# Kernel tuning notes

Measured on AMD Instinct MI355X. Metric: run time of the kernel, lower is better.

## Reference

```python
import jax, jax.numpy as jnp
import numpy as np

B, N, D, H, DEG = 2, 20000, 256, 8, 8
E = N * DEG
EPS = 1e-3  # keras LayerNormalization default epsilon


def layer_norm(x, gamma, beta):
    mu = jnp.mean(x, axis=-1, keepdims=True)
    var = jnp.mean(jnp.square(x - mu), axis=-1, keepdims=True)
    return (x - mu) * jax.lax.rsqrt(var + EPS) * gamma + beta


def setup_inputs() -> dict:
    key = jax.random.key(0)
    ks = jax.random.split(key, 8)
    x = jax.random.normal(ks[0], (B, N, D), dtype=jnp.float32)
    # edge list sorted by source node; every node has DEG out-edges so
    # segment_sum covers all N segments (matches tf.math.segment_sum semantics)
    src = jnp.repeat(jnp.arange(N, dtype=jnp.int64), DEG)
    dst = jax.random.randint(ks[1], (E,), 0, N, dtype=jnp.int64)
    edges = jnp.stack([src, dst], axis=1)  # [E, 2]
    scale = 0.05
    wq = jax.random.normal(ks[2], (D, D), dtype=jnp.float32) * scale
    wk = jax.random.normal(ks[3], (D, D), dtype=jnp.float32) * scale
    wv = jax.random.normal(ks[4], (D, D), dtype=jnp.float32) * scale
    wo = jax.random.normal(ks[5], (D, D), dtype=jnp.float32) * scale
    zeros = jnp.zeros((D,), dtype=jnp.float32)
    ones = jnp.ones((D,), dtype=jnp.float32)
    return {
        "x": x, "edges": edges,
        "wq": wq, "bq": zeros, "wk": wk, "bk": zeros,
        "wv": wv, "bv": zeros, "wo": wo, "bo": zeros,
        "gamma1": ones, "beta1": zeros, "gamma2": ones, "beta2": zeros,
    }


def reference(x, edges, wq, bq, wk, bk, wv, bv, wo, bo, gamma1, beta1, gamma2, beta2):
    b, n, d = x.shape
    h, dh = H, D // H
    xn = layer_norm(x, gamma1, beta1)                      # [B,N,D]
    # QKV projections, split heads, move node axis to front: [N,B,H,dh]
    def proj(w, bias):
        y = (xn @ w + bias).reshape(b, n, h, dh)
        return jnp.transpose(y, (1, 0, 2, 3))
    q, k, v = proj(wq, bq), proj(wk, bk), proj(wv, bv)
    src, dst = edges[:, 0], edges[:, 1]
    q_part = q[src]                                         # [E,B,H,dh]
    k_part = k[dst]
    v_part = v[dst]
    logits = jnp.sum(q_part * k_part, axis=-1, keepdims=True) / jnp.sqrt(
        jnp.asarray(dh, dtype=x.dtype))                     # [E,B,H,1]
    w = jnp.exp(logits)                                     # unnormalized softmax (as in source)
    num = jax.ops.segment_sum(v_part * w, src, num_segments=n)  # [N,B,H,dh]
    den = jax.ops.segment_sum(w, src, num_segments=n)           # [N,B,H,1]
    attn = num / den
    attn = jnp.transpose(attn, (1, 0, 2, 3)).reshape(b, n, d)   # [B,N,D]
    concat = xn + attn                                      # residual uses normed input (source reassigns `inputs`)
    out = layer_norm(concat, gamma2, beta2)
    out = jax.nn.relu(out @ wo + bo)
    return out + concat
```

## Files before the change

kernel.cpp:

```cpp
#include <hip/hip_runtime.h>


typedef __bf16 bf16x8 __attribute__((ext_vector_type(8)));
typedef float  f32x4  __attribute__((ext_vector_type(4)));

__device__ __forceinline__ float bf2f(unsigned short u) {
    union { unsigned int i; float f; } v; v.i = ((unsigned int)u) << 16; return v.f;
}
__device__ __forceinline__ unsigned short f2bf(float f) {
    union { float f; unsigned int i; } v; v.f = f;
    unsigned int x = v.i;
    unsigned int r = (x + 0x7FFFu + ((x >> 16) & 1u)) >> 16;
    return (unsigned short)r;
}

#define NNODE 20000
#define ROWS  40000
#define DMODEL 256

__global__ __launch_bounds__(256) void prep_kernel(
    const float* __restrict__ wq, const float* __restrict__ wk,
    const float* __restrict__ wv, const float* __restrict__ wo,
    const float* __restrict__ bq, const float* __restrict__ bk,
    const float* __restrict__ bv, const float* __restrict__ bo,
    unsigned short* __restrict__ Wqkvt,
    unsigned short* __restrict__ Wot,
    float* __restrict__ biasq,
    float* __restrict__ biaso)
{
    int idx = blockIdx.x * 256 + threadIdx.x;
    if (idx < 768 * 256) {
        int n = idx >> 8, k = idx & 255;
        int sel = n >> 8, nl = n & 255;
        const float* w = (sel == 0) ? wq : (sel == 1) ? wk : wv;
        Wqkvt[idx] = f2bf(w[k * 256 + nl]);
    } else {
        int idx2 = idx - 768 * 256;
        int n = idx2 >> 8, k = idx2 & 255;
        Wot[idx2] = f2bf(wo[k * 256 + n]);
    }
    if (idx < 768) {
        const float* bb = (idx < 256) ? bq : (idx < 512) ? bk : bv;
        biasq[idx] = bb[idx & 255];
    }
    if (idx >= 768 && idx < 1024) biaso[idx - 768] = bo[idx - 768];
}

__global__ __launch_bounds__(256) void ln1_kernel(
    const float* __restrict__ x,
    const float* __restrict__ g1, const float* __restrict__ b1,
    unsigned short* __restrict__ xn)
{
    int wave = threadIdx.x >> 6, lane = threadIdx.x & 63;
    int sub = lane >> 5, hl = lane & 31;
    int m = blockIdx.x * 8 + wave * 2 + sub;
    const float* xp = x + (size_t)m * DMODEL + hl * 8;
    float4 x0 = *(const float4*)xp;
    float4 x1 = *(const float4*)(xp + 4);
    float f[8] = {x0.x, x0.y, x0.z, x0.w, x1.x, x1.y, x1.z, x1.w};
    float s = 0.f, ss = 0.f;
    #pragma unroll
    for (int t = 0; t < 8; ++t) { s += f[t]; ss += f[t]*f[t]; }
    #pragma unroll
    for (int mk = 1; mk < 32; mk <<= 1) { s += __shfl_xor(s, mk); ss += __shfl_xor(ss, mk); }
    float mu  = s * (1.f/256.f);
    float var = ss * (1.f/256.f) - mu*mu;
    float rs  = rsqrtf(var + 1e-3f);
    float4 g0 = *(const float4*)(g1 + hl * 8);
    float4 g1v = *(const float4*)(g1 + hl * 8 + 4);
    float4 b0 = *(const float4*)(b1 + hl * 8);
    float4 b1v = *(const float4*)(b1 + hl * 8 + 4);
    float gg[8] = {g0.x, g0.y, g0.z, g0.w, g1v.x, g1v.y, g1v.z, g1v.w};
    float bb[8] = {b0.x, b0.y, b0.z, b0.w, b1v.x, b1v.y, b1v.z, b1v.w};
    unsigned short o[8];
    #pragma unroll
    for (int t = 0; t < 8; ++t) o[t] = f2bf((f[t] - mu) * rs * gg[t] + bb[t]);
    *(int4*)(xn + (size_t)m * DMODEL + hl * 8) = *(const int4*)o;
}

#define LDS_W 72
#define MFMA_BF16(d, a, b) d = __builtin_amdgcn_mfma_f32_16x16x32_bf16(a, b, d, 0, 0, 0)

template<bool EPI>
__global__ __launch_bounds__(256, 2) void gemm_kernel(
    const unsigned short* __restrict__ A,
    const unsigned short* __restrict__ Bt,
    const float* __restrict__ bias,
    void* __restrict__ C,
    const unsigned short* __restrict__ resid,
    int M, int Ncols)
{
    __shared__ unsigned short As[128 * LDS_W];
    __shared__ unsigned short Bs[128 * LDS_W];
    int tid  = threadIdx.x;
    int wave = tid >> 6, lane = tid & 63;
    int quad = lane >> 4, l16 = lane & 15;
    int m0 = blockIdx.x * 128, n0 = blockIdx.y * 128;
    int wm = (wave >> 1) * 64, wn = (wave & 1) * 64;

    int srow = tid >> 1;
    int sseg = (tid & 1) * 32;
    int arow = m0 + srow; if (arow >= M) arow = M - 1;
    const unsigned short* ArowP = A  + (size_t)arow * 256 + sseg;
    const unsigned short* BrowP = Bt + (size_t)(n0 + srow) * 256 + sseg;
    unsigned short* AsP = &As[srow * LDS_W + sseg];
    unsigned short* BsP = &Bs[srow * LDS_W + sseg];

    f32x4 acc00 = {}, acc01 = {}, acc02 = {}, acc03 = {};
    f32x4 acc10 = {}, acc11 = {}, acc12 = {}, acc13 = {};
    f32x4 acc20 = {}, acc21 = {}, acc22 = {}, acc23 = {};
    f32x4 acc30 = {}, acc31 = {}, acc32 = {}, acc33 = {};

    for (int kt = 0; kt < 4; ++kt) {
        const unsigned short* ap = ArowP + kt * 64;
        const unsigned short* bp = BrowP + kt * 64;
        int4 va0 = *(const int4*)(ap);
        int4 va1 = *(const int4*)(ap + 8);
        int4 va2 = *(const int4*)(ap + 16);
        int4 va3 = *(const int4*)(ap + 24);
        int4 vb0 = *(const int4*)(bp);
        int4 vb1 = *(const int4*)(bp + 8);
        int4 vb2 = *(const int4*)(bp + 16);
        int4 vb3 = *(const int4*)(bp + 24);
        __syncthreads();
        *(int4*)(AsP)      = va0;
        *(int4*)(AsP + 8)  = va1;
        *(int4*)(AsP + 16) = va2;
        *(int4*)(AsP + 24) = va3;
        *(int4*)(BsP)      = vb0;
        *(int4*)(BsP + 8)  = vb1;
        *(int4*)(BsP + 16) = vb2;
        *(int4*)(BsP + 24) = vb3;
        __syncthreads();
        #pragma unroll
        for (int ks = 0; ks < 64; ks += 32) {
            bf16x8 a0 = *(const bf16x8*)&As[(wm +  0 + l16) * LDS_W + ks + quad * 8];
            bf16x8 a1 = *(const bf16x8*)&As[(wm + 16 + l16) * LDS_W + ks + quad * 8];
            bf16x8 a2 = *(const bf16x8*)&As[(wm + 32 + l16) * LDS_W + ks + quad * 8];
            bf16x8 a3 = *(const bf16x8*)&As[(wm + 48 + l16) * LDS_W + ks + quad * 8];
            bf16x8 b0 = *(const bf16x8*)&Bs[(wn +  0 + l16) * LDS_W + ks + quad * 8];
            bf16x8 b1 = *(const bf16x8*)&Bs[(wn + 16 + l16) * LDS_W + ks + quad * 8];
            bf16x8 b2 = *(const bf16x8*)&Bs[(wn + 32 + l16) * LDS_W + ks + quad * 8];
            bf16x8 b3 = *(const bf16x8*)&Bs[(wn + 48 + l16) * LDS_W + ks + quad * 8];
            MFMA_BF16(acc00, a0, b0); MFMA_BF16(acc01, a0, b1);
            MFMA_BF16(acc02, a0, b2); MFMA_BF16(acc03, a0, b3);
            MFMA_BF16(acc10, a1, b0); MFMA_BF16(acc11, a1, b1);
            MFMA_BF16(acc12, a1, b2); MFMA_BF16(acc13, a1, b3);
            MFMA_BF16(acc20, a2, b0); MFMA_BF16(acc21, a2, b1);
            MFMA_BF16(acc22, a2, b2); MFMA_BF16(acc23, a2, b3);
            MFMA_BF16(acc30, a3, b0); MFMA_BF16(acc31, a3, b1);
            MFMA_BF16(acc32, a3, b2); MFMA_BF16(acc33, a3, b3);
        }
    }

#define EPI_STORE(accv, R, CC) do {                                          \
        int col = n0 + wn + (CC) * 16 + l16;                                 \
        float bb = bias[col];                                                \
        int rowb = m0 + wm + (R) * 16 + quad * 4;                            \
        _Pragma("unroll")                                                    \
        for (int rr = 0; rr < 4; ++rr) {                                     \
            int row = rowb + rr;                                             \
            if (row < M) {                                                   \
                float v = (accv)[rr] + bb;                                   \
                if (EPI) {                                                   \
                    v = fmaxf(v, 0.f);                                       \
                    v += bf2f(resid[(size_t)row * 256 + col]);               \
                    ((float*)C)[(size_t)row * Ncols + col] = v;              \
                } else {                                                     \
                    ((unsigned short*)C)[(size_t)row * Ncols + col] = f2bf(v);\
                }                                                            \
            }                                                                \
        }                                                                    \
    } while (0)

    EPI_STORE(acc00, 0, 0); EPI_STORE(acc01, 0, 1); EPI_STORE(acc02, 0, 2); EPI_STORE(acc03, 0, 3);
    EPI_STORE(acc10, 1, 0); EPI_STORE(acc11, 1, 1); EPI_STORE(acc12, 1, 2); EPI_STORE(acc13, 1, 3);
    EPI_STORE(acc20, 2, 0); EPI_STORE(acc21, 2, 1); EPI_STORE(acc22, 2, 2); EPI_STORE(acc23, 2, 3);
    EPI_STORE(acc30, 3, 0); EPI_STORE(acc31, 3, 1); EPI_STORE(acc32, 3, 2); EPI_STORE(acc33, 3, 3);
#undef EPI_STORE
}

__global__ __launch_bounds__(256) void attn_kernel(
    const unsigned short* __restrict__ qkv,
    const int* __restrict__ edges,
    const unsigned short* __restrict__ xn,
    const float* __restrict__ g2, const float* __restrict__ b2,
    unsigned short* __restrict__ concat,
    unsigned short* __restrict__ h2)
{
    int wave = threadIdx.x >> 6, lane = threadIdx.x & 63;
    int i = blockIdx.x * 4 + wave;
    int b = lane >> 5, hl = lane & 31;
    size_t m = (size_t)b * NNODE + i;

    int4 qi = *(const int4*)(qkv + m * 768 + hl * 8);
    const unsigned short* qs = (const unsigned short*)&qi;
    float qf[8];
    #pragma unroll
    for (int t = 0; t < 8; ++t) qf[t] = bf2f(qs[t]);

    int jv = 0;
    if (lane < 8) jv = edges[2 * (i * 8 + lane) + 1];

    float acc[8] = {};
    float den = 0.f;
    const float scale = 0.17677669529663687f;
    #pragma unroll
    for (int e = 0; e < 8; ++e) {
        int j = __shfl(jv, e);
        const unsigned short* kp = qkv + ((size_t)b * NNODE + j) * 768 + 256 + hl * 8;
        int4 ki = *(const int4*)kp;
        int4 vi = *(const int4*)(kp + 256);
        const unsigned short* ks = (const unsigned short*)&ki;
        const unsigned short* vs = (const unsigned short*)&vi;
        float dot = 0.f;
        #pragma unroll
        for (int t = 0; t < 8; ++t) dot += qf[t] * bf2f(ks[t]);
        dot += __shfl_xor(dot, 1);
        dot += __shfl_xor(dot, 2);
        float w = __expf(dot * scale);
        #pragma unroll
        for (int t = 0; t < 8; ++t) acc[t] += w * bf2f(vs[t]);
        den += w;
    }
    float inv = 1.f / den;

    int4 xi = *(const int4*)(xn + m * DMODEL + hl * 8);
    const unsigned short* xs = (const unsigned short*)&xi;
    float c[8], s = 0.f, ss = 0.f;
    #pragma unroll
    for (int t = 0; t < 8; ++t) { c[t] = bf2f(xs[t]) + acc[t] * inv; s += c[t]; ss += c[t]*c[t]; }
    #pragma unroll
    for (int mk = 1; mk < 32; mk <<= 1) { s += __shfl_xor(s, mk); ss += __shfl_xor(ss, mk); }
    float mu  = s * (1.f/256.f);
    float var = ss * (1.f/256.f) - mu*mu;
    float rs  = rsqrtf(var + 1e-3f);

    float4 ga = *(const float4*)(g2 + hl * 8);
    float4 gb = *(const float4*)(g2 + hl * 8 + 4);
    float4 ba = *(const float4*)(b2 + hl * 8);
    float4 bb = *(const float4*)(b2 + hl * 8 + 4);
    float gg[8] = {ga.x, ga.y, ga.z, ga.w, gb.x, gb.y, gb.z, gb.w};
    float bv[8] = {ba.x, ba.y, ba.z, ba.w, bb.x, bb.y, bb.z, bb.w};
    unsigned short oc[8], oh[8];
    #pragma unroll
    for (int t = 0; t < 8; ++t) {
        oc[t] = f2bf(c[t]);
        oh[t] = f2bf((c[t] - mu) * rs * gg[t] + bv[t]);
    }
    *(int4*)(concat + m * DMODEL + hl * 8) = *(const int4*)oc;
    *(int4*)(h2     + m * DMODEL + hl * 8) = *(const int4*)oh;
}

extern "C" void kernel_launch(void* const* d_in, const int* in_sizes, int n_in,
                              void* d_out, int out_size, void* d_ws, size_t ws_size,
                              hipStream_t stream)
{
    const float* x   = (const float*)d_in[0];
    const int* edges = (const int*)d_in[1];
    const float* wq = (const float*)d_in[2];
    const float* bq = (const float*)d_in[3];
    const float* wk = (const float*)d_in[4];
    const float* bk = (const float*)d_in[5];
    const float* wv = (const float*)d_in[6];
    const float* bv = (const float*)d_in[7];
    const float* wo = (const float*)d_in[8];
    const float* bo = (const float*)d_in[9];
    const float* g1 = (const float*)d_in[10];
    const float* b1 = (const float*)d_in[11];
    const float* g2 = (const float*)d_in[12];
    const float* b2 = (const float*)d_in[13];

    char* ws = (char*)d_ws;
    unsigned short* Wqkvt = (unsigned short*)(ws);
    unsigned short* Wot   = (unsigned short*)(ws + 393216);
    float* biasq          = (float*)(ws + 393216 + 131072);
    float* biaso          = (float*)(ws + 393216 + 131072 + 3072);
    size_t off = 393216 + 131072 + 4096;
    unsigned short* xn     = (unsigned short*)(ws + off); off += (size_t)ROWS * DMODEL * 2;
    unsigned short* qkv    = (unsigned short*)(ws + off); off += (size_t)ROWS * 768 * 2;
    unsigned short* concat = (unsigned short*)(ws + off); off += (size_t)ROWS * DMODEL * 2;
    unsigned short* h2     = (unsigned short*)(ws + off); off += (size_t)ROWS * DMODEL * 2;

    prep_kernel<<<1024, 256, 0, stream>>>(wq, wk, wv, wo, bq, bk, bv, bo, Wqkvt, Wot, biasq, biaso);
    ln1_kernel<<<ROWS / 8, 256, 0, stream>>>(x, g1, b1, xn);
    gemm_kernel<false><<<dim3(313, 6), 256, 0, stream>>>(xn, Wqkvt, biasq, qkv, nullptr, ROWS, 768);
    attn_kernel<<<NNODE / 4, 256, 0, stream>>>(qkv, edges, xn, g2, b2, concat, h2);
    gemm_kernel<true><<<dim3(313, 2), 256, 0, stream>>>(h2, Wot, biaso, d_out, concat, ROWS, 256);
}
```

Baseline: 238.9 us.

## Use direct global-to-LDS loads in GEMM and batch gather loads in attention

The GEMM now stages A/B tiles with global_load_lds (direct global-to-LDS DMA) using a 32-wide K slice, doubling the k-loop count. The smaller shared footprint allows a launch-bounds target of three blocks per SM. The attention kernel issues all eight K/V neighbor gathers up front before computing, to expose memory-level parallelism. The LDS layout loses its padding, which risks bank conflicts. There is also no explicit wait on the async loads before the barrier, so correctness depends on the compiler inserting vmcnt waits.

```diff
diff --git a/kernel.cpp b/kernel.cpp
--- a/kernel.cpp
+++ b/kernel.cpp
@@ -12,6 +12,12 @@
     unsigned int x = v.i;
     unsigned int r = (x + 0x7FFFu + ((x >> 16) & 1u)) >> 16;
     return (unsigned short)r;
+}
+__device__ __forceinline__ void async16(const unsigned short* g, unsigned short* l) {
+    __builtin_amdgcn_global_load_lds(
+        (const __attribute__((address_space(1))) unsigned int*)g,
+        (__attribute__((address_space(3))) unsigned int*)l,
+        16, 0, 0);
 }
 
 #define NNODE 20000
@@ -78,11 +84,10 @@
     *(int4*)(xn + (size_t)m * DMODEL + hl * 8) = *(const int4*)o;
 }
 
-#define LDS_W 72
 #define MFMA_BF16(d, a, b) d = __builtin_amdgcn_mfma_f32_16x16x32_bf16(a, b, d, 0, 0, 0)
 
 template<bool EPI>
-__global__ __launch_bounds__(256, 2) void gemm_kernel(
+__global__ __launch_bounds__(256, 3) void gemm_kernel(
     const unsigned short* __restrict__ A,
     const unsigned short* __restrict__ Bt,
     const float* __restrict__ bias,
@@ -90,67 +95,53 @@
     const unsigned short* __restrict__ resid,
     int M, int Ncols)
 {
-    __shared__ unsigned short As[128 * LDS_W];
-    __shared__ unsigned short Bs[128 * LDS_W];
+    __shared__ unsigned short As[128 * 32];
+    __shared__ unsigned short Bs[128 * 32];
     int tid  = threadIdx.x;
     int wave = tid >> 6, lane = tid & 63;
     int quad = lane >> 4, l16 = lane & 15;
     int m0 = blockIdx.x * 128, n0 = blockIdx.y * 128;
     int wm = (wave >> 1) * 64, wn = (wave & 1) * 64;
 
-    int srow = tid >> 1;
-    int sseg = (tid & 1) * 32;
-    int arow = m0 + srow; if (arow >= M) arow = M - 1;
-    const unsigned short* ArowP = A  + (size_t)arow * 256 + sseg;
-    const unsigned short* BrowP = Bt + (size_t)(n0 + srow) * 256 + sseg;
-    unsigned short* AsP = &As[srow * LDS_W + sseg];
-    unsigned short* BsP = &Bs[srow * LDS_W + sseg];
+    int r0 = tid >> 2;
+    int cb = (tid & 3) * 8;
+    int arow0 = m0 + r0;      if (arow0 >= M) arow0 = M - 1;
+    int arow1 = m0 + 64 + r0; if (arow1 >= M) arow1 = M - 1;
+    const unsigned short* Ag0 = A  + (size_t)arow0 * 256 + cb;
+    const unsigned short* Ag1 = A  + (size_t)arow1 * 256 + cb;
+    const unsigned short* Bg0 = Bt + (size_t)(n0 + r0) * 256 + cb;
+    const unsigned short* Bg1 = Bt + (size_t)(n0 + 64 + r0) * 256 + cb;
+    unsigned short* AsW = As + wave * 512;
+    unsigned short* BsW = Bs + wave * 512;
 
     f32x4 acc00 = {}, acc01 = {}, acc02 = {}, acc03 = {};
     f32x4 acc10 = {}, acc11 = {}, acc12 = {}, acc13 = {};
     f32x4 acc20 = {}, acc21 = {}, acc22 = {}, acc23 = {};
     f32x4 acc30 = {}, acc31 = {}, acc32 = {}, acc33 = {};
 
-    for (int kt = 0; kt < 4; ++kt) {
-        const unsigned short* ap = ArowP + kt * 64;
-        const unsigned short* bp = BrowP + kt * 64;
-        int4 va0 = *(const int4*)(ap);
-        int4 va1 = *(const int4*)(ap + 8);
-        int4 va2 = *(const int4*)(ap + 16);
-        int4 va3 = *(const int4*)(ap + 24);
-        int4 vb0 = *(const int4*)(bp);
-        int4 vb1 = *(const int4*)(bp + 8);
-        int4 vb2 = *(const int4*)(bp + 16);
-        int4 vb3 = *(const int4*)(bp + 24);
+    for (int kt = 0; kt < 8; ++kt) {
         __syncthreads();
-        *(int4*)(AsP)      = va0;
-        *(int4*)(AsP + 8)  = va1;
-        *(int4*)(AsP + 16) = va2;
-        *(int4*)(AsP + 24) = va3;
-        *(int4*)(BsP)      = vb0;
-        *(int4*)(BsP + 8)  = vb1;
-        *(int4*)(BsP + 16) = vb2;
-        *(int4*)(BsP + 24) = vb3;
+        async16(Ag0 + kt * 32, AsW);
+        async16(Ag1 + kt * 32, AsW + 2048);
+        async16(Bg0 + kt * 32, BsW);
+        async16(Bg1 + kt * 32, BsW + 2048);
         __syncthreads();
-        #pragma unroll
-        for (int ks = 0; ks < 64; ks += 32) {
-            bf16x8 a0 = *(const bf16x8*)&As[(wm +  0 + l16) * LDS_W + ks + quad * 8];
-            bf16x8 a1 = *(const bf16x8*)&As[(wm + 16 + l16) * LDS_W + ks + quad * 8];
-            bf16x8 a2 = *(const bf16x8*)&As[(wm + 32 + l16) * LDS_W + ks + quad * 8];
-            bf16x8 a3 = *(const bf16x8*)&As[(wm + 48 + l16) * LDS_W + ks + quad * 8];
-            bf16x8 b0 = *(const bf16x8*)&Bs[(wn +  0 + l16) * LDS_W + ks + quad * 8];
-            bf16x8 b1 = *(const bf16x8*)&Bs[(wn + 16 + l16) * LDS_W + ks + quad * 8];
-            bf16x8 b2 = *(const bf16x8*)&Bs[(wn + 32 + l16) * LDS_W + ks + quad * 8];
-            bf16x8 b3 = *(const bf16x8*)&Bs[(wn + 48 + l16) * LDS_W + ks + quad * 8];
-            MFMA_BF16(acc00, a0, b0); MFMA_BF16(acc01, a0, b1);
-            MFMA_BF16(acc02, a0, b2); MFMA_BF16(acc03, a0, b3);
-            MFMA_BF16(acc10, a1, b0); MFMA_BF16(acc11, a1, b1);
-            MFMA_BF16(acc12, a1, b2); MFMA_BF16(acc13, a1, b3);
-            MFMA_BF16(acc20, a2, b0); MFMA_BF16(acc21, a2, b1);
-            MFMA_BF16(acc22, a2, b2); MFMA_BF16(acc23, a2, b3);
-            MFMA_BF16(acc30, a3, b0); MFMA_BF16(acc31, a3, b1);
-            MFMA_BF16(acc32, a3, b2); MFMA_BF16(acc33, a3, b3);
-        }
+        bf16x8 a0 = *(const bf16x8*)&As[(wm +  0 + l16) * 32 + quad * 8];
+        bf16x8 a1 = *(const bf16x8*)&As[(wm + 16 + l16) * 32 + quad * 8];
+        bf16x8 a2 = *(const bf16x8*)&As[(wm + 32 + l16) * 32 + quad * 8];
+        bf16x8 a3 = *(const bf16x8*)&As[(wm + 48 + l16) * 32 + quad * 8];
+        bf16x8 b0 = *(const bf16x8*)&Bs[(wn +  0 + l16) * 32 + quad * 8];
+        bf16x8 b1 = *(const bf16x8*)&Bs[(wn + 16 + l16) * 32 + quad * 8];
+        bf16x8 b2 = *(const bf16x8*)&Bs[(wn + 32 + l16) * 32 + quad * 8];
+        bf16x8 b3 = *(const bf16x8*)&Bs[(wn + 48 + l16) * 32 + quad * 8];
+        MFMA_BF16(acc00, a0, b0); MFMA_BF16(acc01, a0, b1);
+        MFMA_BF16(acc02, a0, b2); MFMA_BF16(acc03, a0, b3);
+        MFMA_BF16(acc10, a1, b0); MFMA_BF16(acc11, a1, b1);
+        MFMA_BF16(acc12, a1, b2); MFMA_BF16(acc13, a1, b3);
+        MFMA_BF16(acc20, a2, b0); MFMA_BF16(acc21, a2, b1);
+        MFMA_BF16(acc22, a2, b2); MFMA_BF16(acc23, a2, b3);
+        MFMA_BF16(acc30, a3, b0); MFMA_BF16(acc31, a3, b1);
+        MFMA_BF16(acc32, a3, b2); MFMA_BF16(acc33, a3, b3);
     }
 
 #define EPI_STORE(accv, R, CC) do {                                          \
@@ -202,27 +193,34 @@
     int jv = 0;
     if (lane < 8) jv = edges[2 * (i * 8 + lane) + 1];
 
+#define KVLOAD(E)                                                                  \
+    int j##E = __shfl(jv, E);                                                      \
+    const unsigned short* kp##E = qkv + ((size_t)b * NNODE + j##E) * 768 + 256 + hl * 8; \
+    int4 KI##E = *(const int4*)(kp##E);                                            \
+    int4 VI##E = *(const int4*)(kp##E + 256);
+    KVLOAD(0) KVLOAD(1) KVLOAD(2) KVLOAD(3)
+    KVLOAD(4) KVLOAD(5) KVLOAD(6) KVLOAD(7)
+#undef KVLOAD
+
     float acc[8] = {};
     float den = 0.f;
     const float scale = 0.17677669529663687f;
-    #pragma unroll
-    for (int e = 0; e < 8; ++e) {
-        int j = __shfl(jv, e);
-        const unsigned short* kp = qkv + ((size_t)b * NNODE + j) * 768 + 256 + hl * 8;
-        int4 ki = *(const int4*)kp;
-        int4 vi = *(const int4*)(kp + 256);
-        const unsigned short* ks = (const unsigned short*)&ki;
-        const unsigned short* vs = (const unsigned short*)&vi;
-        float dot = 0.f;
-        #pragma unroll
-        for (int t = 0; t < 8; ++t) dot += qf[t] * bf2f(ks[t]);
-        dot += __shfl_xor(dot, 1);
-        dot += __shfl_xor(dot, 2);
-        float w = __expf(dot * scale);
-        #pragma unroll
-        for (int t = 0; t < 8; ++t) acc[t] += w * bf2f(vs[t]);
-        den += w;
-    }
+#define EDGE(E) do {                                                         \
+        const unsigned short* ks = (const unsigned short*)&KI##E;            \
+        const unsigned short* vs = (const unsigned short*)&VI##E;            \
+        float dot = 0.f;                                                     \
+        _Pragma("unroll")                                                    \
+        for (int t = 0; t < 8; ++t) dot += qf[t] * bf2f(ks[t]);              \
+        dot += __shfl_xor(dot, 1);                                           \
+        dot += __shfl_xor(dot, 2);               \
+        float w = __expf(dot * scale);                                       \
+        _Pragma("unroll")                                                    \
+        for (int t = 0; t < 8; ++t) acc[t] += w * bf2f(vs[t]);               \
+        den += w;                                                            \
+    } while (0)
+    EDGE(0); EDGE(1); EDGE(2); EDGE(3);
+    EDGE(4); EDGE(5); EDGE(6); EDGE(7);
+#undef EDGE
     float inv = 1.f / den;
 
     int4 xi = *(const int4*)(xn + m * DMODEL + hl * 8);
```

Result: slower. 349.5 us (+46.3%).
